# Optimization experiments

Hardware: AMD Instinct MI355X
Metric: run time of the kernel (lower is better)

The kernel has to match this reference:

```python
import jax, jax.numpy as jnp
import numpy as np

B, S, D, H = 2, 2048, 768, 12
DK = D // H

def setup_inputs() -> dict:
    key = jax.random.key(0)
    ks = jax.random.split(key, 8)
    query = jax.random.normal(ks[0], (B, S, D), dtype=jnp.float32)
    key_t = jax.random.normal(ks[1], (B, S, D), dtype=jnp.float32)
    value = jax.random.normal(ks[2], (B, S, D), dtype=jnp.float32)
    # causal (look-ahead) mask: True above the diagonal -> masked
    mask = jnp.triu(jnp.ones((S, S), dtype=bool), k=1)[None, None]  # (1,1,S,S)
    scale = 1.0 / np.sqrt(D)
    w_q = jax.random.normal(ks[3], (D, D), dtype=jnp.float32) * scale
    w_k = jax.random.normal(ks[4], (D, D), dtype=jnp.float32) * scale
    w_v = jax.random.normal(ks[5], (D, D), dtype=jnp.float32) * scale
    w_o = jax.random.normal(ks[6], (D, D), dtype=jnp.float32) * scale
    return {"query": query, "key": key_t, "value": value, "mask": mask,
            "w_q": w_q, "w_k": w_k, "w_v": w_v, "w_o": w_o}

def reference(query, key, value, mask, w_q, w_k, w_v, w_o):
    b = query.shape[0]
    # nn.Linear(bias=False): y = x @ W.T
    q = (query @ w_q.T).reshape(b, -1, H, DK).transpose(0, 2, 1, 3)  # (B,H,Sq,dk)
    k = (key @ w_k.T).reshape(b, -1, H, DK).transpose(0, 2, 1, 3)    # (B,H,Sk,dk)
    v = (value @ w_v.T).reshape(b, -1, H, DK).transpose(0, 2, 1, 3)  # (B,H,Sk,dk)
    scores = jnp.einsum('bhqd,bhkd->bhqk', q, k) / jnp.sqrt(jnp.float32(DK))
    scores = jnp.where(mask, jnp.float32(-1e9), scores)
    attn_weights = jax.nn.softmax(scores, axis=-1)  # (B,H,Sq,Sk); dropout=0 (eval)
    context = jnp.einsum('bhqk,bhkd->bhqd', attn_weights, v)
    context = context.transpose(0, 2, 1, 3).reshape(b, -1, D)
    output = context @ w_o.T
    return output, attn_weights
```

## Files before the change

kernel.cpp:

```cpp
#include <hip/hip_runtime.h>

#define BATCH 2
#define S_LEN 2048
#define NH 12
#define DMODEL 768

#define N8_BSD (BATCH * S_LEN * DMODEL / 8)
#define N8_DD (DMODEL * DMODEL / 8)

typedef __attribute__((ext_vector_type(8))) short bf16x8;
typedef __attribute__((ext_vector_type(4))) float f32x4;
typedef __attribute__((ext_vector_type(4))) unsigned short us4;

__device__ __forceinline__ unsigned short f2bf(float f) {
  union { float f; unsigned int u; } v; v.f = f;
  unsigned int r = v.u + 0x7fffu + ((v.u >> 16) & 1u);
  return (unsigned short)(r >> 16);
}

__global__ void cvt3_kernel(const float* __restrict__ s0,
                            const float* __restrict__ s1,
                            const float* __restrict__ s2,
                            unsigned short* __restrict__ dst) {
  int i = blockIdx.x * blockDim.x + threadIdx.x;
  int j = i / N8_BSD;
  int k = i - j * N8_BSD;
  const float* s = (j == 0) ? s0 : (j == 1) ? s1 : s2;
  const float4* sp = (const float4*)s;
  float4 a = sp[k * 2], b = sp[k * 2 + 1];
  us4 o0 = { f2bf(a.x), f2bf(a.y), f2bf(a.z), f2bf(a.w) };
  us4 o1 = { f2bf(b.x), f2bf(b.y), f2bf(b.z), f2bf(b.w) };
  us4* d = (us4*)dst;
  d[i * 2] = o0;
  d[i * 2 + 1] = o1;
}

__global__ void cvt4_kernel(const float* __restrict__ s0,
                            const float* __restrict__ s1,
                            const float* __restrict__ s2,
                            const float* __restrict__ s3,
                            unsigned short* __restrict__ dst) {
  int i = blockIdx.x * blockDim.x + threadIdx.x;
  int j = i / N8_DD;
  int k = i - j * N8_DD;
  const float* s = (j == 0) ? s0 : (j == 1) ? s1 : (j == 2) ? s2 : s3;
  const float4* sp = (const float4*)s;
  float4 a = sp[k * 2], b = sp[k * 2 + 1];
  us4 o0 = { f2bf(a.x), f2bf(a.y), f2bf(a.z), f2bf(a.w) };
  us4 o1 = { f2bf(b.x), f2bf(b.y), f2bf(b.z), f2bf(b.w) };
  us4* d = (us4*)dst;
  d[i * 2] = o0;
  d[i * 2 + 1] = o1;
}

__global__ void ctx_reduce(const float* __restrict__ c0,
                           const float* __restrict__ c1,
                           unsigned short* __restrict__ o) {
  int i = blockIdx.x * blockDim.x + threadIdx.x;
  int s = (i / 192) & (S_LEN - 1);
  float4 a = ((const float4*)c0)[i];
  float4 r = a;
  if (s >= 1024) {
    float4 b = ((const float4*)c1)[i];
    r.x += b.x; r.y += b.y; r.z += b.z; r.w += b.w;
  }
  us4 u = { f2bf(r.x), f2bf(r.y), f2bf(r.z), f2bf(r.w) };
  ((us4*)o)[i] = u;
}

#define GLD_LDS16(g, l)                                                    \
  __builtin_amdgcn_global_load_lds(                                        \
      (const __attribute__((address_space(1))) unsigned int*)(g),          \
      (__attribute__((address_space(3))) unsigned int*)(l), 16, 0, 0)

__global__ __launch_bounds__(256, 2)
void gemm_qkv(const unsigned short* __restrict__ Aq,
              const unsigned short* __restrict__ Ak,
              const unsigned short* __restrict__ Av,
              const unsigned short* __restrict__ W3,
              unsigned short* __restrict__ Qs,
              unsigned short* __restrict__ Ks,
              unsigned short* __restrict__ VT) {
  __shared__ unsigned short As[128 * 64];
  __shared__ unsigned short Bs[128 * 64];
  const int m0 = blockIdx.x * 128;
  const int n0g = blockIdx.y * 128;
  const int nblk = n0g / 768;
  const int n0 = n0g - nblk * 768;
  const unsigned short* A = (nblk == 0) ? Aq : (nblk == 1) ? Ak : Av;
  const unsigned short* Bw = W3 + (size_t)n0g * DMODEL;
  const int tid = threadIdx.x, w = tid >> 6, l = tid & 63;
  const int lg = l >> 4, ll = l & 15;
  const int wm = w >> 1, wn = w & 1;
  const int lr = l >> 3, lc = (l & 7) * 8;

  f32x4 acc[4][4];
#pragma unroll
  for (int i = 0; i < 4; ++i)
#pragma unroll
    for (int j = 0; j < 4; ++j) acc[i][j] = (f32x4){0.f, 0.f, 0.f, 0.f};

  for (int k0 = 0; k0 < DMODEL; k0 += 64) {
#pragma unroll
    for (int i = 0; i < 4; ++i) {
      GLD_LDS16(A + (size_t)(m0 + w * 32 + i * 8 + lr) * DMODEL + k0 + lc,
                &As[(w * 32 + i * 8) * 64]);
      GLD_LDS16(Bw + (size_t)(w * 32 + i * 8 + lr) * DMODEL + k0 + lc,
                &Bs[(w * 32 + i * 8) * 64]);
    }
    __syncthreads();
#pragma unroll
    for (int t = 0; t < 2; ++t) {
      bf16x8 af[4], bf[4];
#pragma unroll
      for (int mi = 0; mi < 4; ++mi)
        af[mi] = *(const bf16x8*)&As[(wm * 64 + mi * 16 + ll) * 64 + t * 32 + lg * 8];
#pragma unroll
      for (int ni = 0; ni < 4; ++ni)
        bf[ni] = *(const bf16x8*)&Bs[(wn * 64 + ni * 16 + ll) * 64 + t * 32 + lg * 8];
#pragma unroll
      for (int mi = 0; mi < 4; ++mi)
#pragma unroll
        for (int ni = 0; ni < 4; ++ni)
          acc[mi][ni] = __builtin_amdgcn_mfma_f32_16x16x32_bf16(
              af[mi], bf[ni], acc[mi][ni], 0, 0, 0);
    }
    __syncthreads();
  }

  if (nblk < 2) {
    unsigned short* o = nblk ? Ks : Qs;
    const float sc = nblk ? 1.f : 0.125f;
#pragma unroll
    for (int mi = 0; mi < 4; ++mi)
#pragma unroll
      for (int ni = 0; ni < 4; ++ni) {
        const int col = n0 + wn * 64 + ni * 16 + ll;
        const int rowb = m0 + wm * 64 + mi * 16 + lg * 4;
#pragma unroll
        for (int r = 0; r < 4; ++r)
          o[(size_t)(rowb + r) * 768 + col] = f2bf(acc[mi][ni][r] * sc);
      }
  } else {
#pragma unroll
    for (int mi = 0; mi < 4; ++mi)
#pragma unroll
      for (int ni = 0; ni < 4; ++ni) {
        const int col = n0 + wn * 64 + ni * 16 + ll;
        const int row = m0 + wm * 64 + mi * 16 + lg * 4;
        const int bb = row >> 11, sidx = row & (S_LEN - 1);
        const size_t base =
            ((size_t)(bb * NH + (col >> 6)) * 64 + (col & 63)) * S_LEN + sidx;
        us4 pk = { f2bf(acc[mi][ni][0]), f2bf(acc[mi][ni][1]),
                   f2bf(acc[mi][ni][2]), f2bf(acc[mi][ni][3]) };
        *(us4*)&VT[base] = pk;
      }
  }
}

__global__ __launch_bounds__(256, 2)
void gemm_proj(const unsigned short* __restrict__ A,
               const unsigned short* __restrict__ Bw,
               float* __restrict__ o) {
  __shared__ unsigned short As[128 * 64];
  __shared__ unsigned short Bs[128 * 64];
  const int m0 = blockIdx.x * 128, n0 = blockIdx.y * 128;
  const int tid = threadIdx.x, w = tid >> 6, l = tid & 63;
  const int lg = l >> 4, ll = l & 15;
  const int wm = w >> 1, wn = w & 1;
  const int lr = l >> 3, lc = (l & 7) * 8;

  f32x4 acc[4][4];
#pragma unroll
  for (int i = 0; i < 4; ++i)
#pragma unroll
    for (int j = 0; j < 4; ++j) acc[i][j] = (f32x4){0.f, 0.f, 0.f, 0.f};

  for (int k0 = 0; k0 < DMODEL; k0 += 64) {
#pragma unroll
    for (int i = 0; i < 4; ++i) {
      GLD_LDS16(A + (size_t)(m0 + w * 32 + i * 8 + lr) * DMODEL + k0 + lc,
                &As[(w * 32 + i * 8) * 64]);
      GLD_LDS16(Bw + (size_t)(n0 + w * 32 + i * 8 + lr) * DMODEL + k0 + lc,
                &Bs[(w * 32 + i * 8) * 64]);
    }
    __syncthreads();
#pragma unroll
    for (int t = 0; t < 2; ++t) {
      bf16x8 af[4], bf[4];
#pragma unroll
      for (int mi = 0; mi < 4; ++mi)
        af[mi] = *(const bf16x8*)&As[(wm * 64 + mi * 16 + ll) * 64 + t * 32 + lg * 8];
#pragma unroll
      for (int ni = 0; ni < 4; ++ni)
        bf[ni] = *(const bf16x8*)&Bs[(wn * 64 + ni * 16 + ll) * 64 + t * 32 + lg * 8];
#pragma unroll
      for (int mi = 0; mi < 4; ++mi)
#pragma unroll
        for (int ni = 0; ni < 4; ++ni)
          acc[mi][ni] = __builtin_amdgcn_mfma_f32_16x16x32_bf16(
              af[mi], bf[ni], acc[mi][ni], 0, 0, 0);
    }
    __syncthreads();
  }

#pragma unroll
  for (int mi = 0; mi < 4; ++mi)
#pragma unroll
    for (int ni = 0; ni < 4; ++ni) {
      const int col = n0 + wn * 64 + ni * 16 + ll;
      const int rowb = m0 + wm * 64 + mi * 16 + lg * 4;
#pragma unroll
      for (int r = 0; r < 4; ++r)
        o[(size_t)(rowb + r) * DMODEL + col] = acc[mi][ni][r];
    }
}

#define STAGE_TILE(srcTile, srcStride, ldsT)                                  \
  {                                                                           \
    _Pragma("unroll") for (int j_ = 0; j_ < 2; ++j_) {                        \
      int slot_ = (j_ * 4 + w) * 64 + l;                                      \
      int row_ = slot_ >> 3, c16_ = slot_ & 7;                                \
      GLD_LDS16((srcTile) + (size_t)row_ * (srcStride) +                      \
                    ((c16_ ^ (row_ & 7)) << 3),                               \
                (ldsT) + (j_ * 4 + w) * 512);                                 \
    }                                                                         \
  }

__global__ __launch_bounds__(256, 3)
void attn_ml(const unsigned short* __restrict__ Qp,
             const unsigned short* __restrict__ Kp,
             float2* __restrict__ mlbuf) {
  const int idx = blockIdx.x;
  const int hb = idx >> 5;
  const int qt = 31 - (idx & 31);
  const int h = hb >> 1, b = hb & 1;
  const int tid = threadIdx.x, w = tid >> 6, l = tid & 63;
  const int lg = l >> 4, ll = l & 15;
  __shared__ unsigned short Kt[2][64 * 64];

  const unsigned short* kbp = Kp + (size_t)b * S_LEN * DMODEL + h * 64;
  const int q0 = qt * 64 + w * 16;
  const int nkt = qt + 1;

  bf16x8 qf[2];
  {
    const unsigned short* qb =
        Qp + (size_t)(b * S_LEN + q0 + ll) * DMODEL + h * 64 + lg * 8;
    qf[0] = *(const bf16x8*)qb;
    qf[1] = *(const bf16x8*)(qb + 32);
  }
  int rowg[4];
#pragma unroll
  for (int r = 0; r < 4; ++r) rowg[r] = q0 + lg * 4 + r;

  float m[4], lsum[4];
#pragma unroll
  for (int r = 0; r < 4; ++r) { m[r] = -1e30f; lsum[r] = 0.f; }

  STAGE_TILE(kbp + (size_t)0 * 64 * DMODEL, DMODEL, &Kt[0][0]);
  __syncthreads();

  for (int kt = 0; kt < nkt; ++kt) {
    const int cur = kt & 1;
    if (kt + 1 < nkt)
      STAGE_TILE(kbp + (size_t)(kt + 1) * 64 * DMODEL, DMODEL, &Kt[cur ^ 1][0]);
    bf16x8 kf[8];
#pragma unroll
    for (int t = 0; t < 2; ++t)
#pragma unroll
      for (int nb = 0; nb < 4; ++nb) {
        const int row = nb * 16 + ll;
        kf[t * 4 + nb] = *(const bf16x8*)&Kt[cur][row * 64 +
            (((t * 4 + lg) ^ (row & 7)) << 3)];
      }
    f32x4 sv[4];
#pragma unroll
    for (int nb = 0; nb < 4; ++nb) sv[nb] = (f32x4){0.f, 0.f, 0.f, 0.f};
#pragma unroll
    for (int t = 0; t < 2; ++t)
#pragma unroll
      for (int nb = 0; nb < 4; ++nb)
        sv[nb] = __builtin_amdgcn_mfma_f32_16x16x32_bf16(qf[t], kf[t * 4 + nb],
                                                         sv[nb], 0, 0, 0);
    if (kt == nkt - 1) {
#pragma unroll
      for (int nb = 0; nb < 4; ++nb) {
        const int col = kt * 64 + nb * 16 + ll;
#pragma unroll
        for (int r = 0; r < 4; ++r)
          if (col > rowg[r]) sv[nb][r] = -1e30f;
      }
    }
#pragma unroll
    for (int r = 0; r < 4; ++r) {
      float tm = fmaxf(fmaxf(sv[0][r], sv[1][r]), fmaxf(sv[2][r], sv[3][r]));
      float mn = fmaxf(m[r], tm);
      float te = __expf(sv[0][r] - mn) + __expf(sv[1][r] - mn) +
                 __expf(sv[2][r] - mn) + __expf(sv[3][r] - mn);
      lsum[r] = lsum[r] * __expf(m[r] - mn) + te;
      m[r] = mn;
    }
    __syncthreads();
  }

#pragma unroll
  for (int off = 1; off < 16; off <<= 1)
#pragma unroll
    for (int r = 0; r < 4; ++r) {
      float om = __shfl_xor(m[r], off, 64);
      float ol = __shfl_xor(lsum[r], off, 64);
      float mn = fmaxf(m[r], om);
      lsum[r] = lsum[r] * __expf(m[r] - mn) + ol * __expf(om - mn);
      m[r] = mn;
    }

  if (ll == 0) {
    float2* mlb = mlbuf + (size_t)(b * NH + h) * S_LEN;
#pragma unroll
    for (int r = 0; r < 4; ++r)
      mlb[rowg[r]] = make_float2(m[r], 1.f / lsum[r]);
  }
}

__global__ __launch_bounds__(256, 3)
void attn_p2(const unsigned short* __restrict__ Qp,
             const unsigned short* __restrict__ Kp,
             const unsigned short* __restrict__ VTp,
             const float2* __restrict__ mlbuf,
             float* __restrict__ attnw,
             float* __restrict__ ctx0,
             float* __restrict__ ctx1) {
  const int idx = blockIdx.x;
  const int hb = idx >> 7;
  const int sl = idx & 127;
  const int slot = sl >> 1;
  const int qh = sl & 1;
  const int h = hb >> 1, b = hb & 1;
  int qt, ck;
  if (slot <= 16)      { ck = 0; qt = 15 + slot; }
  else if (slot == 17) { ck = 1; qt = 31; }
  else if (slot < 48)  { int u = slot - 18; int k = 15 - (u >> 1);
                         if (u & 1) { ck = 1; qt = k + 15; } else { ck = 0; qt = k - 1; } }
  else                 { ck = 1; qt = slot - 48; }

  const int ktlo = ck * 16;
  const int kthi = (qt < ktlo + 15) ? qt : (ktlo + 15);
  const bool hasval = (ktlo <= qt);

  const int tid = threadIdx.x, w = tid >> 6, l = tid & 63;
  const int lg = l >> 4, ll = l & 15;
  __shared__ float pf32[4][32 * 64];
  float* pfw = &pf32[w][0];

  const unsigned short* kbp = Kp + (size_t)b * S_LEN * DMODEL + h * 64;
  const unsigned short* vbp = VTp + ((size_t)(b * NH + h)) * 64 * S_LEN;
  float* pbase = attnw + ((size_t)(b * NH + h)) * S_LEN * S_LEN;
  const int q0g = qt * 64 + qh * 32;

  if (hasval) {
    bf16x8 qf[2][2];
#pragma unroll
    for (int rb = 0; rb < 2; ++rb) {
      const unsigned short* qb =
          Qp + (size_t)(b * S_LEN + q0g + rb * 16 + ll) * DMODEL + h * 64 + lg * 8;
      qf[rb][0] = *(const bf16x8*)qb;
      qf[rb][1] = *(const bf16x8*)(qb + 32);
    }
    float m16[2][4], li16[2][4];
    {
      const float2* mlb = mlbuf + (size_t)(b * NH + h) * S_LEN;
#pragma unroll
      for (int rb = 0; rb < 2; ++rb)
#pragma unroll
        for (int r = 0; r < 4; ++r) {
          float2 t = mlb[q0g + rb * 16 + lg * 4 + r];
          m16[rb][r] = t.x;
          li16[rb][r] = t.y;
        }
    }

    f32x4 cacc[2][4];
#pragma unroll
    for (int rb = 0; rb < 2; ++rb)
#pragma unroll
      for (int vb = 0; vb < 4; ++vb) cacc[rb][vb] = (f32x4){0.f, 0.f, 0.f, 0.f};

    for (int kt = ktlo + w; kt <= kthi; kt += 4) {
      bf16x8 kf[2][4];
#pragma unroll
      for (int t = 0; t < 2; ++t)
#pragma unroll
        for (int nb = 0; nb < 4; ++nb)
          kf[t][nb] = *(const bf16x8*)(kbp +
              (size_t)(kt * 64 + nb * 16 + ll) * DMODEL + t * 32 + lg * 8);
      f32x4 sv[2][4];
#pragma unroll
      for (int rb = 0; rb < 2; ++rb)
#pragma unroll
        for (int nb = 0; nb < 4; ++nb) sv[rb][nb] = (f32x4){0.f, 0.f, 0.f, 0.f};
#pragma unroll
      for (int t = 0; t < 2; ++t)
#pragma unroll
        for (int rb = 0; rb < 2; ++rb)
#pragma unroll
          for (int nb = 0; nb < 4; ++nb)
            sv[rb][nb] = __builtin_amdgcn_mfma_f32_16x16x32_bf16(
                qf[rb][t], kf[t][nb], sv[rb][nb], 0, 0, 0);
#pragma unroll
      for (int nb = 0; nb < 4; ++nb) {
        const int col = kt * 64 + nb * 16 + ll;
#pragma unroll
        for (int rb = 0; rb < 2; ++rb)
#pragma unroll
          for (int r = 0; r < 4; ++r) {
            const int row = q0g + rb * 16 + lg * 4 + r;
            float p = (col <= row)
                          ? __expf(sv[rb][nb][r] - m16[rb][r]) * li16[rb][r]
                          : 0.f;
            pfw[(rb * 16 + lg * 4 + r) * 64 +
                ((nb * 16 + ll) ^ ((lg & 1) << 4))] = p;
          }
      }
#pragma unroll
      for (int t = 0; t < 2; ++t) {
        bf16x8 pfr[2];
#pragma unroll
        for (int rb = 0; rb < 2; ++rb) {
          const int row = rb * 16 + ll;
          const int c0 = (t * 32 + lg * 8) ^ (((ll >> 2) & 1) << 4);
          f32x4 lo = *(const f32x4*)&pfw[row * 64 + c0];
          f32x4 hi = *(const f32x4*)&pfw[row * 64 + c0 + 4];
          union { us4 hh2[2]; bf16x8 v; } u;
          u.hh2[0] = (us4){ f2bf(lo[0]), f2bf(lo[1]), f2bf(lo[2]), f2bf(lo[3]) };
          u.hh2[1] = (us4){ f2bf(hi[0]), f2bf(hi[1]), f2bf(hi[2]), f2bf(hi[3]) };
          pfr[rb] = u.v;
        }
        bf16x8 vf[4];
#pragma unroll
        for (int vb = 0; vb < 4; ++vb)
          vf[vb] = *(const bf16x8*)(vbp +
              (size_t)(vb * 16 + ll) * S_LEN + kt * 64 + t * 32 + lg * 8);
#pragma unroll
        for (int rb = 0; rb < 2; ++rb)
#pragma unroll
          for (int vb = 0; vb < 4; ++vb)
            cacc[rb][vb] = __builtin_amdgcn_mfma_f32_16x16x32_bf16(
                pfr[rb], vf[vb], cacc[rb][vb], 0, 0, 0);
      }
#pragma unroll
      for (int ps = 0; ps < 8; ++ps) {
        const int lrow = ps * 4 + lg;
        const int cb = (ll * 4) ^ ((ps & 1) << 4);
        f32x4 pv = *(const f32x4*)&pfw[lrow * 64 + cb];
        __builtin_nontemporal_store(
            pv, (f32x4*)&pbase[(size_t)(q0g + lrow) * S_LEN + kt * 64 + ll * 4]);
      }
    }

#pragma unroll
    for (int rb = 0; rb < 2; ++rb)
#pragma unroll
      for (int vb = 0; vb < 4; ++vb)
#pragma unroll
        for (int r = 0; r < 4; ++r)
          pfw[(rb * 16 + lg * 4 + r) * 64 +
              ((vb * 16 + ll) ^ ((lg & 1) << 4))] = cacc[rb][vb][r];
    __syncthreads();
    float* co = ck ? ctx1 : ctx0;
#pragma unroll
    for (int ps2 = 0; ps2 < 2; ++ps2) {
      const int lrow = w * 8 + ps2 * 4 + lg;
      const int cb = (ll * 4) ^ ((ps2 & 1) << 4);
      f32x4 s0 = *(const f32x4*)&pf32[0][lrow * 64 + cb];
      f32x4 s1 = *(const f32x4*)&pf32[1][lrow * 64 + cb];
      f32x4 s2 = *(const f32x4*)&pf32[2][lrow * 64 + cb];
      f32x4 s3 = *(const f32x4*)&pf32[3][lrow * 64 + cb];
      f32x4 sm = (s0 + s1) + (s2 + s3);
      *(f32x4*)&co[(size_t)(b * S_LEN + q0g + lrow) * DMODEL + h * 64 + ll * 4] = sm;
    }
  }

  const int zs = ((qt + 1) * 64 > ktlo * 64) ? (qt + 1) * 64 : ktlo * 64;
  const int ze = (ktlo + 16) * 64;
  if (zs < ze) {
    f32x4 z = (f32x4){0.f, 0.f, 0.f, 0.f};
    for (int rr = 0; rr < 8; ++rr) {
      float* dst = pbase + (size_t)(q0g + w * 8 + rr) * S_LEN;
      for (int c = zs + l * 4; c < ze; c += 256)
        __builtin_nontemporal_store(z, (f32x4*)(dst + c));
    }
  }
}

extern "C" void kernel_launch(void* const* d_in, const int* in_sizes, int n_in,
                              void* d_out, int out_size, void* d_ws, size_t ws_size,
                              hipStream_t stream) {
  const float* q_in = (const float*)d_in[0];
  const float* k_in = (const float*)d_in[1];
  const float* v_in = (const float*)d_in[2];
  const float* wq = (const float*)d_in[4];
  const float* wk = (const float*)d_in[5];
  const float* wv = (const float*)d_in[6];
  const float* wo = (const float*)d_in[7];

  const int BSD = BATCH * S_LEN * DMODEL;
  const int DD = DMODEL * DMODEL;
  const int M = BATCH * S_LEN;

  char* ws = (char*)d_ws;
  unsigned short* qbf = (unsigned short*)ws;  ws += (size_t)BSD * 2;
  unsigned short* kbf = (unsigned short*)ws;  ws += (size_t)BSD * 2;
  unsigned short* vbf = (unsigned short*)ws;  ws += (size_t)BSD * 2;
  unsigned short* wqb = (unsigned short*)ws;  ws += (size_t)DD * 2;
  unsigned short* wkb = (unsigned short*)ws;  ws += (size_t)DD * 2;
  unsigned short* wvb = (unsigned short*)ws;  ws += (size_t)DD * 2;
  unsigned short* wob = (unsigned short*)ws;  ws += (size_t)DD * 2;
  unsigned short* Qs  = (unsigned short*)ws;  ws += (size_t)BSD * 2;
  unsigned short* Ks  = (unsigned short*)ws;  ws += (size_t)BSD * 2;
  unsigned short* VT  = (unsigned short*)ws;  ws += (size_t)BSD * 2;
  unsigned short* ctx = (unsigned short*)ws;  ws += (size_t)BSD * 2;
  float* ctx0 = (float*)ws;                   ws += (size_t)BSD * 4;
  float* ctx1 = (float*)ws;                   ws += (size_t)BSD * 4;
  float2* mlbuf = (float2*)ws;                ws += (size_t)M * NH * sizeof(float2);
  (void)wkb; (void)wvb;

  float* out_proj = (float*)d_out;
  float* attnw = (float*)d_out + BSD;

  cvt3_kernel<<<3 * N8_BSD / 256, 256, 0, stream>>>(q_in, k_in, v_in, qbf);
  cvt4_kernel<<<4 * N8_DD / 256, 256, 0, stream>>>(wq, wk, wv, wo, wqb);

  gemm_qkv<<<dim3(M / 128, 2304 / 128), 256, 0, stream>>>(qbf, kbf, vbf, wqb,
                                                          Qs, Ks, VT);

  attn_ml<<<32 * NH * BATCH, 256, 0, stream>>>(Qs, Ks, mlbuf);
  attn_p2<<<128 * NH * BATCH, 256, 0, stream>>>(Qs, Ks, VT, mlbuf, attnw,
                                                ctx0, ctx1);
  ctx_reduce<<<BSD / 4 / 256, 256, 0, stream>>>(ctx0, ctx1, ctx);

  gemm_proj<<<dim3(M / 128, DMODEL / 128), 256, 0, stream>>>(ctx, wob, out_proj);
}
```

Baseline: 187.2 us.

## Drop key-split in attention pass 2 and fuse context reduce; merge convert kernels

The second attention pass no longer splits each query tile's key range into two chunks with separate fp32 context buffers. Each block now handles the full causal key range for a 32-row slice and writes bf16 context directly, which removes the ctx_reduce kernel and the fp32 context round trip. The two fp32-to-bf16 convert kernels are also merged into one launch. In exchange the grid halves and per-block work becomes unbalanced: late query tiles take up to 32 key tiles, ordered largest-first, which may lengthen the tail.

```diff
diff --git a/kernel.cpp b/kernel.cpp
--- a/kernel.cpp
+++ b/kernel.cpp
@@ -18,54 +18,37 @@
   return (unsigned short)(r >> 16);
 }
 
-__global__ void cvt3_kernel(const float* __restrict__ s0,
-                            const float* __restrict__ s1,
-                            const float* __restrict__ s2,
-                            unsigned short* __restrict__ dst) {
+__global__ void cvt_all(const float* __restrict__ q,
+                        const float* __restrict__ k_,
+                        const float* __restrict__ v,
+                        const float* __restrict__ wq,
+                        const float* __restrict__ wk,
+                        const float* __restrict__ wv,
+                        const float* __restrict__ wo,
+                        unsigned short* __restrict__ dqkv,
+                        unsigned short* __restrict__ dw) {
   int i = blockIdx.x * blockDim.x + threadIdx.x;
-  int j = i / N8_BSD;
-  int k = i - j * N8_BSD;
-  const float* s = (j == 0) ? s0 : (j == 1) ? s1 : s2;
-  const float4* sp = (const float4*)s;
-  float4 a = sp[k * 2], b = sp[k * 2 + 1];
+  const float4* sp;
+  us4* d;
+  if (i < 3 * N8_BSD) {
+    int j = i / N8_BSD;
+    int kl = i - j * N8_BSD;
+    const float* s = (j == 0) ? q : (j == 1) ? k_ : v;
+    sp = (const float4*)s + kl * 2;
+    d = (us4*)dqkv + (size_t)i * 2;
+  } else {
+    int t = i - 3 * N8_BSD;
+    int j = t / N8_DD;
+    int kl = t - j * N8_DD;
+    const float* s = (j == 0) ? wq : (j == 1) ? wk : (j == 2) ? wv : wo;
+    sp = (const float4*)s + kl * 2;
+    d = (us4*)dw + (size_t)t * 2;
+  }
+  float4 a = sp[0], b = sp[1];
   us4 o0 = { f2bf(a.x), f2bf(a.y), f2bf(a.z), f2bf(a.w) };
   us4 o1 = { f2bf(b.x), f2bf(b.y), f2bf(b.z), f2bf(b.w) };
-  us4* d = (us4*)dst;
-  d[i * 2] = o0;
-  d[i * 2 + 1] = o1;
-}
-
-__global__ void cvt4_kernel(const float* __restrict__ s0,
-                            const float* __restrict__ s1,
-                            const float* __restrict__ s2,
-                            const float* __restrict__ s3,
-                            unsigned short* __restrict__ dst) {
-  int i = blockIdx.x * blockDim.x + threadIdx.x;
-  int j = i / N8_DD;
-  int k = i - j * N8_DD;
-  const float* s = (j == 0) ? s0 : (j == 1) ? s1 : (j == 2) ? s2 : s3;
-  const float4* sp = (const float4*)s;
-  float4 a = sp[k * 2], b = sp[k * 2 + 1];
-  us4 o0 = { f2bf(a.x), f2bf(a.y), f2bf(a.z), f2bf(a.w) };
-  us4 o1 = { f2bf(b.x), f2bf(b.y), f2bf(b.z), f2bf(b.w) };
-  us4* d = (us4*)dst;
-  d[i * 2] = o0;
-  d[i * 2 + 1] = o1;
-}
-
-__global__ void ctx_reduce(const float* __restrict__ c0,
-                           const float* __restrict__ c1,
-                           unsigned short* __restrict__ o) {
-  int i = blockIdx.x * blockDim.x + threadIdx.x;
-  int s = (i / 192) & (S_LEN - 1);
-  float4 a = ((const float4*)c0)[i];
-  float4 r = a;
-  if (s >= 1024) {
-    float4 b = ((const float4*)c1)[i];
-    r.x += b.x; r.y += b.y; r.z += b.z; r.w += b.w;
-  }
-  us4 u = { f2bf(r.x), f2bf(r.y), f2bf(r.z), f2bf(r.w) };
-  ((us4*)o)[i] = u;
+  d[0] = o0;
+  d[1] = o1;
 }
 
 #define GLD_LDS16(g, l)                                                    \
@@ -329,24 +312,13 @@
              const unsigned short* __restrict__ VTp,
              const float2* __restrict__ mlbuf,
              float* __restrict__ attnw,
-             float* __restrict__ ctx0,
-             float* __restrict__ ctx1) {
+             unsigned short* __restrict__ ctx) {
   const int idx = blockIdx.x;
-  const int hb = idx >> 7;
-  const int sl = idx & 127;
-  const int slot = sl >> 1;
+  const int hb = idx >> 6;
+  const int sl = idx & 63;
+  const int qt = 31 - (sl >> 1);
   const int qh = sl & 1;
   const int h = hb >> 1, b = hb & 1;
-  int qt, ck;
-  if (slot <= 16)      { ck = 0; qt = 15 + slot; }
-  else if (slot == 17) { ck = 1; qt = 31; }
-  else if (slot < 48)  { int u = slot - 18; int k = 15 - (u >> 1);
-                         if (u & 1) { ck = 1; qt = k + 15; } else { ck = 0; qt = k - 1; } }
-  else                 { ck = 1; qt = slot - 48; }
-
-  const int ktlo = ck * 16;
-  const int kthi = (qt < ktlo + 15) ? qt : (ktlo + 15);
-  const bool hasval = (ktlo <= qt);
 
   const int tid = threadIdx.x, w = tid >> 6, l = tid & 63;
   const int lg = l >> 4, ll = l & 15;
@@ -358,136 +330,133 @@
   float* pbase = attnw + ((size_t)(b * NH + h)) * S_LEN * S_LEN;
   const int q0g = qt * 64 + qh * 32;
 
-  if (hasval) {
-    bf16x8 qf[2][2];
-#pragma unroll
-    for (int rb = 0; rb < 2; ++rb) {
-      const unsigned short* qb =
-          Qp + (size_t)(b * S_LEN + q0g + rb * 16 + ll) * DMODEL + h * 64 + lg * 8;
-      qf[rb][0] = *(const bf16x8*)qb;
-      qf[rb][1] = *(const bf16x8*)(qb + 32);
-    }
-    float m16[2][4], li16[2][4];
-    {
-      const float2* mlb = mlbuf + (size_t)(b * NH + h) * S_LEN;
+  bf16x8 qf[2][2];
+#pragma unroll
+  for (int rb = 0; rb < 2; ++rb) {
+    const unsigned short* qb =
+        Qp + (size_t)(b * S_LEN + q0g + rb * 16 + ll) * DMODEL + h * 64 + lg * 8;
+    qf[rb][0] = *(const bf16x8*)qb;
+    qf[rb][1] = *(const bf16x8*)(qb + 32);
+  }
+  float m16[2][4], li16[2][4];
+  {
+    const float2* mlb = mlbuf + (size_t)(b * NH + h) * S_LEN;
+#pragma unroll
+    for (int rb = 0; rb < 2; ++rb)
+#pragma unroll
+      for (int r = 0; r < 4; ++r) {
+        float2 t = mlb[q0g + rb * 16 + lg * 4 + r];
+        m16[rb][r] = t.x;
+        li16[rb][r] = t.y;
+      }
+  }
+
+  f32x4 cacc[2][4];
+#pragma unroll
+  for (int rb = 0; rb < 2; ++rb)
+#pragma unroll
+    for (int vb = 0; vb < 4; ++vb) cacc[rb][vb] = (f32x4){0.f, 0.f, 0.f, 0.f};
+
+  for (int kt = w; kt <= qt; kt += 4) {
+    bf16x8 kf[2][4];
+#pragma unroll
+    for (int t = 0; t < 2; ++t)
+#pragma unroll
+      for (int nb = 0; nb < 4; ++nb)
+        kf[t][nb] = *(const bf16x8*)(kbp +
+            (size_t)(kt * 64 + nb * 16 + ll) * DMODEL + t * 32 + lg * 8);
+    f32x4 sv[2][4];
+#pragma unroll
+    for (int rb = 0; rb < 2; ++rb)
+#pragma unroll
+      for (int nb = 0; nb < 4; ++nb) sv[rb][nb] = (f32x4){0.f, 0.f, 0.f, 0.f};
+#pragma unroll
+    for (int t = 0; t < 2; ++t)
 #pragma unroll
       for (int rb = 0; rb < 2; ++rb)
 #pragma unroll
+        for (int nb = 0; nb < 4; ++nb)
+          sv[rb][nb] = __builtin_amdgcn_mfma_f32_16x16x32_bf16(
+              qf[rb][t], kf[t][nb], sv[rb][nb], 0, 0, 0);
+#pragma unroll
+    for (int nb = 0; nb < 4; ++nb) {
+      const int col = kt * 64 + nb * 16 + ll;
+#pragma unroll
+      for (int rb = 0; rb < 2; ++rb)
+#pragma unroll
         for (int r = 0; r < 4; ++r) {
-          float2 t = mlb[q0g + rb * 16 + lg * 4 + r];
-          m16[rb][r] = t.x;
-          li16[rb][r] = t.y;
+          const int row = q0g + rb * 16 + lg * 4 + r;
+          float p = (col <= row)
+                        ? __expf(sv[rb][nb][r] - m16[rb][r]) * li16[rb][r]
+                        : 0.f;
+          pfw[(rb * 16 + lg * 4 + r) * 64 +
+              ((nb * 16 + ll) ^ ((lg & 1) << 4))] = p;
         }
     }
-
-    f32x4 cacc[2][4];
-#pragma unroll
-    for (int rb = 0; rb < 2; ++rb)
-#pragma unroll
-      for (int vb = 0; vb < 4; ++vb) cacc[rb][vb] = (f32x4){0.f, 0.f, 0.f, 0.f};
-
-    for (int kt = ktlo + w; kt <= kthi; kt += 4) {
-      bf16x8 kf[2][4];
-#pragma unroll
-      for (int t = 0; t < 2; ++t)
-#pragma unroll
-        for (int nb = 0; nb < 4; ++nb)
-          kf[t][nb] = *(const bf16x8*)(kbp +
-              (size_t)(kt * 64 + nb * 16 + ll) * DMODEL + t * 32 + lg * 8);
-      f32x4 sv[2][4];
+#pragma unroll
+    for (int t = 0; t < 2; ++t) {
+      bf16x8 pfr[2];
+#pragma unroll
+      for (int rb = 0; rb < 2; ++rb) {
+        const int row = rb * 16 + ll;
+        const int c0 = (t * 32 + lg * 8) ^ (((ll >> 2) & 1) << 4);
+        f32x4 lo = *(const f32x4*)&pfw[row * 64 + c0];
+        f32x4 hi = *(const f32x4*)&pfw[row * 64 + c0 + 4];
+        union { us4 hh2[2]; bf16x8 v; } u;
+        u.hh2[0] = (us4){ f2bf(lo[0]), f2bf(lo[1]), f2bf(lo[2]), f2bf(lo[3]) };
+        u.hh2[1] = (us4){ f2bf(hi[0]), f2bf(hi[1]), f2bf(hi[2]), f2bf(hi[3]) };
+        pfr[rb] = u.v;
+      }
+      bf16x8 vf[4];
+#pragma unroll
+      for (int vb = 0; vb < 4; ++vb)
+        vf[vb] = *(const bf16x8*)(vbp +
+            (size_t)(vb * 16 + ll) * S_LEN + kt * 64 + t * 32 + lg * 8);
 #pragma unroll
       for (int rb = 0; rb < 2; ++rb)
 #pragma unroll
-        for (int nb = 0; nb < 4; ++nb) sv[rb][nb] = (f32x4){0.f, 0.f, 0.f, 0.f};
-#pragma unroll
-      for (int t = 0; t < 2; ++t)
-#pragma unroll
-        for (int rb = 0; rb < 2; ++rb)
-#pragma unroll
-          for (int nb = 0; nb < 4; ++nb)
-            sv[rb][nb] = __builtin_amdgcn_mfma_f32_16x16x32_bf16(
-                qf[rb][t], kf[t][nb], sv[rb][nb], 0, 0, 0);
-#pragma unroll
-      for (int nb = 0; nb < 4; ++nb) {
-        const int col = kt * 64 + nb * 16 + ll;
-#pragma unroll
-        for (int rb = 0; rb < 2; ++rb)
-#pragma unroll
-          for (int r = 0; r < 4; ++r) {
-            const int row = q0g + rb * 16 + lg * 4 + r;
-            float p = (col <= row)
-                          ? __expf(sv[rb][nb][r] - m16[rb][r]) * li16[rb][r]
-                          : 0.f;
-            pfw[(rb * 16 + lg * 4 + r) * 64 +
-                ((nb * 16 + ll) ^ ((lg & 1) << 4))] = p;
-          }
-      }
-#pragma unroll
-      for (int t = 0; t < 2; ++t) {
-        bf16x8 pfr[2];
-#pragma unroll
-        for (int rb = 0; rb < 2; ++rb) {
-          const int row = rb * 16 + ll;
-          const int c0 = (t * 32 + lg * 8) ^ (((ll >> 2) & 1) << 4);
-          f32x4 lo = *(const f32x4*)&pfw[row * 64 + c0];
-          f32x4 hi = *(const f32x4*)&pfw[row * 64 + c0 + 4];
-          union { us4 hh2[2]; bf16x8 v; } u;
-          u.hh2[0] = (us4){ f2bf(lo[0]), f2bf(lo[1]), f2bf(lo[2]), f2bf(lo[3]) };
-          u.hh2[1] = (us4){ f2bf(hi[0]), f2bf(hi[1]), f2bf(hi[2]), f2bf(hi[3]) };
-          pfr[rb] = u.v;
-        }
-        bf16x8 vf[4];
-#pragma unroll
         for (int vb = 0; vb < 4; ++vb)
-          vf[vb] = *(const bf16x8*)(vbp +
-              (size_t)(vb * 16 + ll) * S_LEN + kt * 64 + t * 32 + lg * 8);
-#pragma unroll
-        for (int rb = 0; rb < 2; ++rb)
-#pragma unroll
-          for (int vb = 0; vb < 4; ++vb)
-            cacc[rb][vb] = __builtin_amdgcn_mfma_f32_16x16x32_bf16(
-                pfr[rb], vf[vb], cacc[rb][vb], 0, 0, 0);
-      }
-#pragma unroll
-      for (int ps = 0; ps < 8; ++ps) {
-        const int lrow = ps * 4 + lg;
-        const int cb = (ll * 4) ^ ((ps & 1) << 4);
-        f32x4 pv = *(const f32x4*)&pfw[lrow * 64 + cb];
-        __builtin_nontemporal_store(
-            pv, (f32x4*)&pbase[(size_t)(q0g + lrow) * S_LEN + kt * 64 + ll * 4]);
-      }
-    }
-
-#pragma unroll
-    for (int rb = 0; rb < 2; ++rb)
-#pragma unroll
-      for (int vb = 0; vb < 4; ++vb)
-#pragma unroll
-        for (int r = 0; r < 4; ++r)
-          pfw[(rb * 16 + lg * 4 + r) * 64 +
-              ((vb * 16 + ll) ^ ((lg & 1) << 4))] = cacc[rb][vb][r];
-    __syncthreads();
-    float* co = ck ? ctx1 : ctx0;
-#pragma unroll
-    for (int ps2 = 0; ps2 < 2; ++ps2) {
-      const int lrow = w * 8 + ps2 * 4 + lg;
-      const int cb = (ll * 4) ^ ((ps2 & 1) << 4);
-      f32x4 s0 = *(const f32x4*)&pf32[0][lrow * 64 + cb];
-      f32x4 s1 = *(const f32x4*)&pf32[1][lrow * 64 + cb];
-      f32x4 s2 = *(const f32x4*)&pf32[2][lrow * 64 + cb];
-      f32x4 s3 = *(const f32x4*)&pf32[3][lrow * 64 + cb];
-      f32x4 sm = (s0 + s1) + (s2 + s3);
-      *(f32x4*)&co[(size_t)(b * S_LEN + q0g + lrow) * DMODEL + h * 64 + ll * 4] = sm;
-    }
-  }
-
-  const int zs = ((qt + 1) * 64 > ktlo * 64) ? (qt + 1) * 64 : ktlo * 64;
-  const int ze = (ktlo + 16) * 64;
-  if (zs < ze) {
+          cacc[rb][vb] = __builtin_amdgcn_mfma_f32_16x16x32_bf16(
+              pfr[rb], vf[vb], cacc[rb][vb], 0, 0, 0);
+    }
+#pragma unroll
+    for (int ps = 0; ps < 8; ++ps) {
+      const int lrow = ps * 4 + lg;
+      const int cb = (ll * 4) ^ ((ps & 1) << 4);
+      f32x4 pv = *(const f32x4*)&pfw[lrow * 64 + cb];
+      __builtin_nontemporal_store(
+          pv, (f32x4*)&pbase[(size_t)(q0g + lrow) * S_LEN + kt * 64 + ll * 4]);
+    }
+  }
+
+#pragma unroll
+  for (int rb = 0; rb < 2; ++rb)
+#pragma unroll
+    for (int vb = 0; vb < 4; ++vb)
+#pragma unroll
+      for (int r = 0; r < 4; ++r)
+        pfw[(rb * 16 + lg * 4 + r) * 64 +
+            ((vb * 16 + ll) ^ ((lg & 1) << 4))] = cacc[rb][vb][r];
+  __syncthreads();
+#pragma unroll
+  for (int ps2 = 0; ps2 < 2; ++ps2) {
+    const int lrow = w * 8 + ps2 * 4 + lg;
+    const int cb = (ll * 4) ^ ((ps2 & 1) << 4);
+    f32x4 s0 = *(const f32x4*)&pf32[0][lrow * 64 + cb];
+    f32x4 s1 = *(const f32x4*)&pf32[1][lrow * 64 + cb];
+    f32x4 s2 = *(const f32x4*)&pf32[2][lrow * 64 + cb];
+    f32x4 s3 = *(const f32x4*)&pf32[3][lrow * 64 + cb];
+    f32x4 sm = (s0 + s1) + (s2 + s3);
+    us4 pk = { f2bf(sm[0]), f2bf(sm[1]), f2bf(sm[2]), f2bf(sm[3]) };
+    *(us4*)&ctx[(size_t)(b * S_LEN + q0g + lrow) * DMODEL + h * 64 + ll * 4] = pk;
+  }
+
+  const int zs = (qt + 1) * 64;
+  if (zs < S_LEN) {
     f32x4 z = (f32x4){0.f, 0.f, 0.f, 0.f};
     for (int rr = 0; rr < 8; ++rr) {
       float* dst = pbase + (size_t)(q0g + w * 8 + rr) * S_LEN;
-      for (int c = zs + l * 4; c < ze; c += 256)
+      for (int c = zs + l * 4; c < S_LEN; c += 256)
         __builtin_nontemporal_store(z, (f32x4*)(dst + c));
     }
   }
@@ -520,24 +489,20 @@
   unsigned short* Ks  = (unsigned short*)ws;  ws += (size_t)BSD * 2;
   unsigned short* VT  = (unsigned short*)ws;  ws += (size_t)BSD * 2;
   unsigned short* ctx = (unsigned short*)ws;  ws += (size_t)BSD * 2;
-  float* ctx0 = (float*)ws;                   ws += (size_t)BSD * 4;
-  float* ctx1 = (float*)ws;                   ws += (size_t)BSD * 4;
   float2* mlbuf = (float2*)ws;                ws += (size_t)M * NH * sizeof(float2);
   (void)wkb; (void)wvb;
 
   float* out_proj = (float*)d_out;
   float* attnw = (float*)d_out + BSD;
 
-  cvt3_kernel<<<3 * N8_BSD / 256, 256, 0, stream>>>(q_in, k_in, v_in, qbf);
-  cvt4_kernel<<<4 * N8_DD / 256, 256, 0, stream>>>(wq, wk, wv, wo, wqb);
+  cvt_all<<<(3 * N8_BSD + 4 * N8_DD) / 256, 256, 0, stream>>>(
+      q_in, k_in, v_in, wq, wk, wv, wo, qbf, wqb);
 
   gemm_qkv<<<dim3(M / 128, 2304 / 128), 256, 0, stream>>>(qbf, kbf, vbf, wqb,
                                                           Qs, Ks, VT);
 
   attn_ml<<<32 * NH * BATCH, 256, 0, stream>>>(Qs, Ks, mlbuf);
-  attn_p2<<<128 * NH * BATCH, 256, 0, stream>>>(Qs, Ks, VT, mlbuf, attnw,
-                                                ctx0, ctx1);
-  ctx_reduce<<<BSD / 4 / 256, 256, 0, stream>>>(ctx0, ctx1, ctx);
+  attn_p2<<<64 * NH * BATCH, 256, 0, stream>>>(Qs, Ks, VT, mlbuf, attnw, ctx);
 
   gemm_proj<<<dim3(M / 128, DMODEL / 128), 256, 0, stream>>>(ctx, wob, out_proj);
 }
```

Measured after the change: 202.3 us. 8.1% more time.
